# Performance work log

Measured on AMD Instinct MI355X. Metric: run time of the kernel, lower is better.

## Reference

```python
import jax, jax.numpy as jnp
import numpy as np

B, L, V, D, N, K = 8, 512, 50257, 1024, 1024, 256


def setup_inputs() -> dict:
    key = jax.random.key(0)
    ks = jax.random.split(key, 8)
    s = 0.02
    return {
        "input_ids": jax.random.randint(ks[0], (B, L), 0, V, dtype=jnp.int32),
        "emb_inp": jax.random.normal(ks[1], (V, D), jnp.float32) * s,
        "W_ih": jax.random.normal(ks[2], (3 * D, D), jnp.float32) * s,   # rows ordered [r|z|n] like torch GRU
        "W_hh": jax.random.normal(ks[3], (3 * D, D), jnp.float32) * s,
        "b_ih": jnp.zeros((3 * D,), jnp.float32),
        "b_hh": jnp.zeros((3 * D,), jnp.float32),
        "W_A": jax.random.normal(ks[4], (N * K, D), jnp.float32) * s,    # ctx_to_A weight
        "b_A": jnp.zeros((N * K,), jnp.float32),
        "emb_geom": jax.random.normal(ks[5], (V, N), jnp.float32) * s,
    }


def reference(input_ids, emb_inp, W_ih, W_hh, b_ih, b_hh, W_A, b_A, emb_geom):
    # token embedding: (B, L, D)
    x = emb_inp[input_ids]
    # precompute input-side GRU gates once: (B, L, 3D)
    gi = jnp.einsum('bld,gd->blg', x, W_ih) + b_ih

    def step(h, gi_t):
        gh = h @ W_hh.T + b_hh                       # (B, 3D)
        ir, iz, i_n = jnp.split(gi_t, 3, axis=-1)
        hr, hz, h_n = jnp.split(gh, 3, axis=-1)
        r = jax.nn.sigmoid(ir + hr)
        z = jax.nn.sigmoid(iz + hz)
        n = jnp.tanh(i_n + r * h_n)
        h_new = (1.0 - z) * n + z * h                # torch GRU update
        return h_new, None

    h0 = jnp.zeros((x.shape[0], D), x.dtype)
    ctx_vec, _ = jax.lax.scan(step, h0, jnp.swapaxes(gi, 0, 1))  # final hidden (B, D)

    # context -> subspace basis U: (B, n, k)
    U = (ctx_vec @ W_A.T + b_A).reshape(-1, N, K)

    # scores[b,v] = e_v^T (U U^T) e_v == ||U^T e_v||^2  (rank-k rewrite, same math)
    Ue = jnp.einsum('vn,bnk->bvk', emb_geom, U)      # (B, V, K)
    logits = jnp.sum(Ue * Ue, axis=-1)               # (B, V)
    return logits
```

## Files before the change

### kernel.cpp

```cpp
#include <hip/hip_runtime.h>

#define D 1024
#define G3 3072
#define NV 50257
#define NU 1024
#define KU 256
#define TOKROWS 4096
#define SCL 256.0f
#define ISCL2 (1.0f / 65536.0f)
#define ISCL4 (1.0f / 4294967296.0f)

typedef __attribute__((ext_vector_type(8))) _Float16 half8;
typedef __attribute__((ext_vector_type(4))) _Float16 half4;
typedef __attribute__((ext_vector_type(4))) float f32x4;
typedef __attribute__((ext_vector_type(4))) unsigned u32x4;

#define GLDS16(gp, lp) __builtin_amdgcn_global_load_lds( \
    (const __attribute__((address_space(1))) void*)(const void*)(gp), \
    (__attribute__((address_space(3))) void*)(void*)(lp), 16, 0, 0)

static __device__ __forceinline__ float sigmoidf_(float x) {
  return 1.0f / (1.0f + __expf(-x));
}
static __device__ __forceinline__ float tanhf_(float x) {
  float e = __expf(2.0f * x);
  return 1.0f - 2.0f / (e + 1.0f);
}

__global__ __launch_bounds__(256) void k_prep(
    const int* __restrict__ ids, const float* __restrict__ emb,
    const float* __restrict__ Wih,
    _Float16* __restrict__ xh, _Float16* __restrict__ xl,
    _Float16* __restrict__ wh, _Float16* __restrict__ wl)
{
  int t = threadIdx.x;
  int wg = blockIdx.x;
  const float* src;
  _Float16 *dh, *dl;
  if (wg < TOKROWS) {
    src = emb + (size_t)ids[wg] * D;
    dh = xh + (size_t)wg * D; dl = xl + (size_t)wg * D;
  } else {
    int r = wg - TOKROWS;
    src = Wih + (size_t)r * D;
    dh = wh + (size_t)r * D; dl = wl + (size_t)r * D;
  }
  f32x4 v = ((const f32x4*)src)[t];
  half4 h, l;
#pragma unroll
  for (int j = 0; j < 4; ++j) {
    float vs = v[j] * SCL;
    _Float16 hi = (_Float16)vs;
    h[j] = hi;
    l[j] = (_Float16)(vs - (float)hi);
  }
  *(half4*)(dh + t * 4) = h;
  *(half4*)(dl + t * 4) = l;
}

__global__ __launch_bounds__(256) void k_gi(
    const _Float16* __restrict__ Ah, const _Float16* __restrict__ Al,
    const _Float16* __restrict__ Bh, const _Float16* __restrict__ Bl,
    const float* __restrict__ bih, float* __restrict__ gi)
{
  __shared__ _Float16 Ash[128 * 64];
  __shared__ _Float16 Asl[128 * 64];
  __shared__ _Float16 Bsh[128 * 64];
  __shared__ _Float16 Bsl[128 * 64];
  int tid = threadIdx.x;
  int bm = blockIdx.x, bn = blockIdx.y;
  int lane = tid & 63, w = tid >> 6;
  int nl = lane & 15, q = lane >> 4;
  int wr = w >> 1, wc = w & 1;
  f32x4 zero = {0.f, 0.f, 0.f, 0.f};
  f32x4 acc[4][4];
#pragma unroll
  for (int i = 0; i < 4; i++)
#pragma unroll
    for (int j = 0; j < 4; j++) acc[i][j] = zero;
  int srow_in = tid >> 3;
  int cg = ((tid & 7) ^ (srow_in & 7)) * 8;
  for (int kc = 0; kc < 16; ++kc) {
    __syncthreads();
#pragma unroll
    for (int s = 0; s < 4; ++s) {
      size_t go = ((size_t)(bm * 128 + s * 32 + srow_in)) * D + kc * 64 + cg;
      size_t go2 = ((size_t)(bn * 128 + s * 32 + srow_in)) * D + kc * 64 + cg;
      int lb = s * 2048 + w * 512;
      GLDS16(Ah + go, Ash + lb);
      GLDS16(Al + go, Asl + lb);
      GLDS16(Bh + go2, Bsh + lb);
      GLDS16(Bl + go2, Bsl + lb);
    }
    __syncthreads();
    half8 afh[4][2], afl[4][2], bfh[4][2], bfl[4][2];
#pragma unroll
    for (int mt = 0; mt < 4; ++mt) {
      int R = wr * 64 + mt * 16 + nl;
#pragma unroll
      for (int kt = 0; kt < 2; ++kt) {
        int o = R * 64 + ((kt * 4 + q) ^ (R & 7)) * 8;
        afh[mt][kt] = *(const half8*)(Ash + o);
        afl[mt][kt] = *(const half8*)(Asl + o);
      }
    }
#pragma unroll
    for (int nt = 0; nt < 4; ++nt) {
      int R = wc * 64 + nt * 16 + nl;
#pragma unroll
      for (int kt = 0; kt < 2; ++kt) {
        int o = R * 64 + ((kt * 4 + q) ^ (R & 7)) * 8;
        bfh[nt][kt] = *(const half8*)(Bsh + o);
        bfl[nt][kt] = *(const half8*)(Bsl + o);
      }
    }
#pragma unroll
    for (int mt = 0; mt < 4; ++mt)
#pragma unroll
      for (int nt = 0; nt < 4; ++nt)
#pragma unroll
        for (int kt = 0; kt < 2; ++kt) {
          acc[mt][nt] = __builtin_amdgcn_mfma_f32_16x16x32_f16(afh[mt][kt], bfh[nt][kt], acc[mt][nt], 0, 0, 0);
          acc[mt][nt] = __builtin_amdgcn_mfma_f32_16x16x32_f16(afh[mt][kt], bfl[nt][kt], acc[mt][nt], 0, 0, 0);
          acc[mt][nt] = __builtin_amdgcn_mfma_f32_16x16x32_f16(afl[mt][kt], bfh[nt][kt], acc[mt][nt], 0, 0, 0);
        }
  }
#pragma unroll
  for (int mt = 0; mt < 4; ++mt)
#pragma unroll
    for (int nt = 0; nt < 4; ++nt) {
      int col = bn * 128 + wc * 64 + nt * 16 + nl;
      float bv = bih[col];
#pragma unroll
      for (int i = 0; i < 4; i++) {
        int row = bm * 128 + wr * 64 + mt * 16 + q * 4 + i;
        gi[(size_t)row * G3 + col] = acc[mt][nt][i] * ISCL2 + bv;
      }
    }
}

__global__ void k_init(unsigned* __restrict__ rec32)
{
  int t = threadIdx.x;
  for (int i = t; i < 32768; i += 256) rec32[i] = 0u;
}

__global__ __launch_bounds__(384) void k_gru(
    const float* __restrict__ Whh, const float* __restrict__ gi,
    const float* __restrict__ bhh, unsigned* __restrict__ hrec,
    float* __restrict__ ctx)
{
  int tid = threadIdx.x;
  int wid = blockIdx.x;
  int w = tid >> 6;
  int g = w >> 1;
  int kh = w & 1;
  int lane = tid & 63, nl = lane & 15, q = lane >> 4;
  __shared__ _Float16 hs[16 * 1024];
  __shared__ float gp[6][3][8][17];

  half8 bwh[16], bwl[16];
  {
    const float* wrow = Whh + ((size_t)(g * 1024 + wid * 16 + nl)) * D + kh * 512;
#pragma unroll
    for (int kt = 0; kt < 16; ++kt) {
      const f32x4* p = (const f32x4*)(wrow + kt * 32 + q * 8);
      f32x4 v0 = p[0], v1 = p[1];
      half8 h, l;
#pragma unroll
      for (int j = 0; j < 4; ++j) {
        float s0 = v0[j] * SCL;
        _Float16 h0 = (_Float16)s0;
        h[j] = h0; l[j] = (_Float16)(s0 - (float)h0);
        float s1 = v1[j] * SCL;
        _Float16 h1 = (_Float16)s1;
        h[j + 4] = h1; l[j + 4] = (_Float16)(s1 - (float)h1);
      }
      bwh[kt] = h; bwl[kt] = l;
    }
  }

  int m = tid >> 3, np = (tid & 7) * 2;
  int d0 = wid * 16 + np;
  float hr0 = 0.f, hr1 = 0.f;
  float bh[6] = {0, 0, 0, 0, 0, 0};
  if (tid < 64) {
#pragma unroll
    for (int gg = 0; gg < 3; ++gg) {
      bh[gg * 2] = bhh[gg * 1024 + d0];
      bh[gg * 2 + 1] = bhh[gg * 1024 + d0 + 1];
    }
  }
  f32x4 zero = {0, 0, 0, 0};

  for (int step = 0; step < 512; ++step) {
    float gi6[6] = {0, 0, 0, 0, 0, 0};
    if (tid < 64) {
      const float* gpt = gi + ((size_t)(m * 512 + step)) * G3 + d0;
#pragma unroll
      for (int gg = 0; gg < 3; ++gg) {
        gi6[gg * 2] = gpt[gg * 1024];
        gi6[gg * 2 + 1] = gpt[gg * 1024 + 1];
      }
    }

    {
      unsigned want = (unsigned)step;
      const u32x4* rb = (const u32x4*)hrec + (size_t)(step & 1) * 4096;
      u32x4 rv[11];
      unsigned need = 0;
#pragma unroll
      for (int k = 0; k < 11; ++k) {
        int r = tid + k * 384;
        if (r < 4096) need |= (1u << k);
      }
      while (need) {
        unsigned mm = need;
#pragma unroll
        for (int k = 0; k < 11; ++k)
          if (mm & (1u << k)) {
            int r = tid + k * 384;
            asm volatile("global_load_dwordx4 %0, %1, off sc0 sc1"
                         : "=v"(rv[k]) : "v"(rb + r));
          }
        asm volatile("s_waitcnt vmcnt(0)" ::: "memory");
#pragma unroll
        for (int k = 0; k < 11; ++k)
          if ((mm & (1u << k)) && rv[k][2] == want) need &= ~(1u << k);
      }
      __builtin_amdgcn_sched_barrier(0);
#pragma unroll
      for (int k = 0; k < 11; ++k) {
        int r = tid + k * 384;
        if (r < 4096) {
          int w2 = r >> 6, l2 = r & 63;
          int m2 = l2 >> 3;
          int d = (w2 << 4) + ((l2 & 7) << 1);
          int chunk = d >> 3, wi = d & 7;
          int sw = chunk ^ (m2 & 7);
          *(unsigned*)&hs[((m2 * 128 + sw) << 3) + wi] = rv[k][0];
          *(unsigned*)&hs[(((m2 + 8) * 128 + sw) << 3) + wi] = rv[k][1];
        }
      }
    }
    __syncthreads();

    half8 av[16];
#pragma unroll
    for (int kt = 0; kt < 16; ++kt) {
      int chunk = kh * 64 + kt * 4 + q;
      av[kt] = *(const half8*)&hs[(size_t)(nl * 128 + (chunk ^ (nl & 7))) * 8];
    }
    f32x4 ac1 = zero, ac2 = zero;
#pragma unroll
    for (int kt = 0; kt < 16; ++kt) {
      ac1 = __builtin_amdgcn_mfma_f32_16x16x32_f16(av[kt], bwh[kt], ac1, 0, 0, 0);
      ac2 = __builtin_amdgcn_mfma_f32_16x16x32_f16(av[kt], bwl[kt], ac2, 0, 0, 0);
    }
    if (q < 2) {
#pragma unroll
      for (int i = 0; i < 4; i++) {
        gp[w][0][q * 4 + i][nl] = ac1[i];
        gp[w][2][q * 4 + i][nl] = ac2[i];
      }
    } else {
#pragma unroll
      for (int i = 0; i < 4; i++) gp[w][1][(q - 2) * 4 + i][nl] = ac1[i];
    }
    __syncthreads();
    if (tid < 64) {
      float gh[6];
#pragma unroll
      for (int g2 = 0; g2 < 3; ++g2) {
        float s0 = 0.f, s1 = 0.f;
#pragma unroll
        for (int k2 = 0; k2 < 2; ++k2) {
          int wv = g2 * 2 + k2;
#pragma unroll
          for (int s = 0; s < 3; ++s) {
            s0 += gp[wv][s][m][np];
            s1 += gp[wv][s][m][np + 1];
          }
        }
        gh[g2 * 2] = s0 * ISCL2;
        gh[g2 * 2 + 1] = s1 * ISCL2;
      }
      float r0_ = sigmoidf_(gi6[0] + gh[0] + bh[0]);
      float r1_ = sigmoidf_(gi6[1] + gh[1] + bh[1]);
      float z0_ = sigmoidf_(gi6[2] + gh[2] + bh[2]);
      float z1_ = sigmoidf_(gi6[3] + gh[3] + bh[3]);
      float n0_ = tanhf_(gi6[4] + r0_ * (gh[4] + bh[4]));
      float n1_ = tanhf_(gi6[5] + r1_ * (gh[5] + bh[5]));
      float h0_ = (1.f - z0_) * n0_ + z0_ * hr0;
      float h1_ = (1.f - z1_) * n1_ + z1_ * hr1;
      hr0 = h0_; hr1 = h1_;
      float s0 = h0_ * SCL, s1 = h1_ * SCL;
      _Float16 h0h = (_Float16)s0, h1h = (_Float16)s1;
      _Float16 h0l = (_Float16)(s0 - (float)h0h), h1l = (_Float16)(s1 - (float)h1h);
      u32x4 rec;
      rec[0] = (unsigned)__builtin_bit_cast(unsigned short, h0h) |
               ((unsigned)__builtin_bit_cast(unsigned short, h1h) << 16);
      rec[1] = (unsigned)__builtin_bit_cast(unsigned short, h0l) |
               ((unsigned)__builtin_bit_cast(unsigned short, h1l) << 16);
      rec[2] = (unsigned)(step + 1);
      rec[3] = 0u;
      u32x4* dst = (u32x4*)hrec + ((size_t)((step + 1) & 1) * 4096 + wid * 64 + tid);
      asm volatile("global_store_dwordx4 %0, %1, off sc0 sc1"
                   :: "v"(dst), "v"(rec) : "memory");
      if (step == 511) {
        ctx[m * D + d0] = h0_;
        ctx[m * D + d0 + 1] = h1_;
      }
    }
  }
}

__global__ __launch_bounds__(256) void k_u(
    const float* __restrict__ WA, const float* __restrict__ bA,
    const float* __restrict__ ctx, _Float16* __restrict__ Uth,
    _Float16* __restrict__ Utl)
{
  __shared__ float As[128 * 32];
  __shared__ float cx[8][1032];
  int tid = threadIdx.x;
  int RB = blockIdx.x;
#pragma unroll
  for (int jj = 0; jj < 8; ++jj) {
    int e = tid * 32 + jj * 4;
    *(f32x4*)&cx[e >> 10][e & 1023] = *(const f32x4*)(ctx + e);
  }
  float acc[4] = {0.f, 0.f, 0.f, 0.f};
  int b = tid & 7, rq = tid >> 3;
  float* AsW = As + (tid >> 6) * 256;
  int sr = tid >> 3;
  int sc = (tid & 7) * 4;
  __syncthreads();
  for (int kc = 0; kc < 32; ++kc) {
    __syncthreads();
    const float* gsrc = WA + ((size_t)(RB * 128 + sr)) * D + kc * 32 + sc;
    GLDS16(gsrc, AsW);
    GLDS16(gsrc + 32 * D, AsW + 1024);
    GLDS16(gsrc + 64 * D, AsW + 2048);
    GLDS16(gsrc + 96 * D, AsW + 3072);
    __syncthreads();
    f32x4 cxr[8];
#pragma unroll
    for (int kk = 0; kk < 8; ++kk) cxr[kk] = *(const f32x4*)&cx[b][kc * 32 + kk * 4];
#pragma unroll
    for (int r = 0; r < 4; ++r) {
      const float* ap = As + (rq * 4 + r) * 32;
      float s = 0.f;
#pragma unroll
      for (int kk = 0; kk < 8; ++kk) {
        f32x4 a = *(const f32x4*)(ap + kk * 4);
        f32x4 c = cxr[kk];
        s += a[0] * c[0] + a[1] * c[1] + a[2] * c[2] + a[3] * c[3];
      }
      acc[r] += s;
    }
  }
#pragma unroll
  for (int r = 0; r < 4; ++r) {
    int R = RB * 128 + rq * 4 + r;
    float v = (acc[r] + bA[R]) * SCL;
    int n_u = R >> 8, k_u = R & 255;
    _Float16 hi = (_Float16)v;
    size_t o = ((size_t)(b * 256 + k_u)) * NU + n_u;
    Uth[o] = hi;
    Utl[o] = (_Float16)(v - (float)hi);
  }
}

__global__ __launch_bounds__(512, 2) void k_logits(
    const float* __restrict__ eg, const _Float16* __restrict__ Uth,
    const _Float16* __restrict__ Utl, float* __restrict__ out)
{
  __shared__ _Float16 Ash[128 * 40];
  __shared__ _Float16 Asl[128 * 40];
  __shared__ float lacc[8][128];
  int tid = threadIdx.x;
  int v0 = blockIdx.x * 128;
  int lane = tid & 63, w = tid >> 6, nl = lane & 15, q = lane >> 4;
  int bq = w & 3, wk = w >> 2;
  for (int i = tid; i < 1024; i += 512) ((float*)lacc)[i] = 0.f;
  int sr = tid >> 2;
  int sc = (tid & 3) * 8;
  int vr = v0 + sr;
  if (vr >= NV) vr = NV - 1;
  const float* asrc = eg + (size_t)vr * NU;
  f32x4 zero = {0, 0, 0, 0};
  __syncthreads();
  for (int kg = 0; kg < 8; ++kg) {
    f32x4 acc[2][8];
#pragma unroll
    for (int b = 0; b < 2; ++b)
#pragma unroll
      for (int mt = 0; mt < 8; ++mt) acc[b][mt] = zero;
    for (int nc = 0; nc < 32; ++nc) {
      __syncthreads();
      {
        const f32x4* p = (const f32x4*)(asrc + nc * 32 + sc);
        f32x4 u0 = p[0];
        f32x4 u1 = p[1];
        half8 h, l;
#pragma unroll
        for (int j = 0; j < 4; ++j) {
          float s0 = u0[j] * SCL;
          _Float16 h0 = (_Float16)s0;
          h[j] = h0; l[j] = (_Float16)(s0 - (float)h0);
          float s1 = u1[j] * SCL;
          _Float16 h1 = (_Float16)s1;
          h[j + 4] = h1; l[j + 4] = (_Float16)(s1 - (float)h1);
        }
        *(half8*)(Ash + sr * 40 + sc) = h;
        *(half8*)(Asl + sr * 40 + sc) = l;
      }
      __syncthreads();
      half8 bfh0, bfl0, bfh1, bfl1;
      {
        int bb0 = bq * 2;
        size_t o0 = ((size_t)(bb0 * 256 + kg * 32 + wk * 16 + nl)) * NU + nc * 32 + q * 8;
        size_t o1 = o0 + (size_t)256 * NU;
        bfh0 = *(const half8*)(Uth + o0);
        bfl0 = *(const half8*)(Utl + o0);
        bfh1 = *(const half8*)(Uth + o1);
        bfl1 = *(const half8*)(Utl + o1);
      }
      __builtin_amdgcn_s_setprio(1);
#pragma unroll
      for (int c = 0; c < 2; ++c) {
        half8 afh[4], afl[4];
#pragma unroll
        for (int mt = 0; mt < 4; ++mt) {
          int row = (c * 4 + mt) * 16 + nl;
          afh[mt] = *(const half8*)(Ash + row * 40 + q * 8);
          afl[mt] = *(const half8*)(Asl + row * 40 + q * 8);
        }
#pragma unroll
        for (int mt = 0; mt < 4; ++mt) {
          int g = c * 4 + mt;
          acc[0][g] = __builtin_amdgcn_mfma_f32_16x16x32_f16(afh[mt], bfh0, acc[0][g], 0, 0, 0);
          acc[0][g] = __builtin_amdgcn_mfma_f32_16x16x32_f16(afh[mt], bfl0, acc[0][g], 0, 0, 0);
          acc[0][g] = __builtin_amdgcn_mfma_f32_16x16x32_f16(afl[mt], bfh0, acc[0][g], 0, 0, 0);
          acc[1][g] = __builtin_amdgcn_mfma_f32_16x16x32_f16(afh[mt], bfh1, acc[1][g], 0, 0, 0);
          acc[1][g] = __builtin_amdgcn_mfma_f32_16x16x32_f16(afh[mt], bfl1, acc[1][g], 0, 0, 0);
          acc[1][g] = __builtin_amdgcn_mfma_f32_16x16x32_f16(afl[mt], bfh1, acc[1][g], 0, 0, 0);
        }
      }
      __builtin_amdgcn_s_setprio(0);
    }
#pragma unroll
    for (int b = 0; b < 2; ++b) {
      int bb = bq * 2 + b;
#pragma unroll
      for (int mt = 0; mt < 8; ++mt) {
#pragma unroll
        for (int i = 0; i < 4; ++i) {
          float s = acc[b][mt][i] * acc[b][mt][i];
          s += __shfl_xor(s, 1);
          s += __shfl_xor(s, 2);
          s += __shfl_xor(s, 4);
          s += __shfl_xor(s, 8);
          if (nl == 0) atomicAdd(&lacc[bb][mt * 16 + q * 4 + i], s);
        }
      }
    }
  }
  __syncthreads();
  if (tid < 128) {
    int v = v0 + tid;
    if (v < NV) {
#pragma unroll
      for (int b = 0; b < 8; ++b) out[(size_t)b * NV + v] = lacc[b][tid] * ISCL4;
    }
  }
}

extern "C" void kernel_launch(void* const* d_in, const int* in_sizes, int n_in,
                              void* d_out, int out_size, void* d_ws, size_t ws_size,
                              hipStream_t stream)
{
  (void)in_sizes; (void)n_in; (void)out_size; (void)ws_size;
  const int* ids = (const int*)d_in[0];
  const float* emb = (const float*)d_in[1];
  const float* Wih = (const float*)d_in[2];
  const float* Whh = (const float*)d_in[3];
  const float* bih = (const float*)d_in[4];
  const float* bhh = (const float*)d_in[5];
  const float* WA = (const float*)d_in[6];
  const float* bA = (const float*)d_in[7];
  const float* eg = (const float*)d_in[8];
  float* out = (float*)d_out;

  char* ws = (char*)d_ws;
  size_t off = 0;
  auto take = [&](size_t bytes) -> char* {
    char* p = ws + off;
    off += (bytes + 255) & ~(size_t)255;
    return p;
  };
  float* gi32 = (float*)take((size_t)4096 * 3072 * 4);
  char* xregion = take((size_t)4096 * 1024 * 2 * 2);
  _Float16* xh = (_Float16*)xregion;
  _Float16* xl = xh + (size_t)4096 * 1024;
  _Float16* wh = (_Float16*)take((size_t)3072 * 1024 * 2);
  _Float16* wl = (_Float16*)take((size_t)3072 * 1024 * 2);
  unsigned* hrec = (unsigned*)take((size_t)2 * 4096 * 16);
  float* ctx = (float*)take((size_t)8 * 1024 * 4);
  _Float16* Uth = (_Float16*)xregion;
  _Float16* Utl = Uth + (size_t)8 * 256 * 1024;

  k_prep<<<dim3(7168), dim3(256), 0, stream>>>(ids, emb, Wih, xh, xl, wh, wl);
  k_gi<<<dim3(32, 24), dim3(256), 0, stream>>>(xh, xl, wh, wl, bih, gi32);
  k_init<<<dim3(1), dim3(256), 0, stream>>>(hrec);
  k_gru<<<dim3(64), dim3(384), 0, stream>>>(Whh, gi32, bhh, hrec, ctx);
  k_u<<<dim3(2048), dim3(256), 0, stream>>>(WA, bA, ctx, Uth, Utl);
  k_logits<<<dim3(393), dim3(512), 0, stream>>>(eg, Uth, Utl, out);
}
```

Baseline: 2.964 ms.

## Register-prefetch next tile of emb_geom and U in k_logits main loop

Loads the next iteration's emb_geom slice and U fragments into registers while the current tile is converted and multiplied, so global load latency overlaps the MFMA work. Barriers now wait only on LDS (lgkmcnt) rather than all memory, so the in-flight prefetches do not stall them. Launch bounds are relaxed from 2 to 1 blocks per CU to make room for the extra live registers, which may lower occupancy.

Measured after the change: 3.064 ms. +3.4%, slower.

```diff
diff --git a/kernel.cpp b/kernel.cpp
--- a/kernel.cpp
+++ b/kernel.cpp
@@ -18,6 +18,12 @@
 #define GLDS16(gp, lp) __builtin_amdgcn_global_load_lds( \
     (const __attribute__((address_space(1))) void*)(const void*)(gp), \
     (__attribute__((address_space(3))) void*)(void*)(lp), 16, 0, 0)
+
+#define LBAR() do { \
+    asm volatile("s_waitcnt lgkmcnt(0)" ::: "memory"); \
+    __builtin_amdgcn_s_barrier(); \
+    __builtin_amdgcn_sched_barrier(0); \
+  } while (0)
 
 static __device__ __forceinline__ float sigmoidf_(float x) {
   return 1.0f / (1.0f + __expf(-x));
@@ -371,7 +377,7 @@
   }
 }
 
-__global__ __launch_bounds__(512, 2) void k_logits(
+__global__ __launch_bounds__(512, 1) void k_logits(
     const float* __restrict__ eg, const _Float16* __restrict__ Uth,
     const _Float16* __restrict__ Utl, float* __restrict__ out)
 {
@@ -389,7 +395,15 @@
   if (vr >= NV) vr = NV - 1;
   const float* asrc = eg + (size_t)vr * NU;
   f32x4 zero = {0, 0, 0, 0};
-  __syncthreads();
+  int bb0 = bq * 2;
+  f32x4 eu0 = *(const f32x4*)(asrc + sc);
+  f32x4 eu1 = *(const f32x4*)(asrc + sc + 4);
+  size_t ob = ((size_t)(bb0 * 256 + wk * 16 + nl)) * NU + q * 8;
+  half8 pbh0 = *(const half8*)(Uth + ob);
+  half8 pbl0 = *(const half8*)(Utl + ob);
+  half8 pbh1 = *(const half8*)(Uth + ob + (size_t)256 * NU);
+  half8 pbl1 = *(const half8*)(Utl + ob + (size_t)256 * NU);
+
   for (int kg = 0; kg < 8; ++kg) {
     f32x4 acc[2][8];
 #pragma unroll
@@ -397,35 +411,37 @@
 #pragma unroll
       for (int mt = 0; mt < 8; ++mt) acc[b][mt] = zero;
     for (int nc = 0; nc < 32; ++nc) {
-      __syncthreads();
+      LBAR();
+      f32x4 ceu0 = eu0, ceu1 = eu1;
+      half8 bh0 = pbh0, bl0 = pbl0, bh1 = pbh1, bl1 = pbl1;
       {
-        const f32x4* p = (const f32x4*)(asrc + nc * 32 + sc);
-        f32x4 u0 = p[0];
-        f32x4 u1 = p[1];
         half8 h, l;
 #pragma unroll
         for (int j = 0; j < 4; ++j) {
-          float s0 = u0[j] * SCL;
+          float s0 = ceu0[j] * SCL;
           _Float16 h0 = (_Float16)s0;
           h[j] = h0; l[j] = (_Float16)(s0 - (float)h0);
-          float s1 = u1[j] * SCL;
+          float s1 = ceu1[j] * SCL;
           _Float16 h1 = (_Float16)s1;
           h[j + 4] = h1; l[j + 4] = (_Float16)(s1 - (float)h1);
         }
         *(half8*)(Ash + sr * 40 + sc) = h;
         *(half8*)(Asl + sr * 40 + sc) = l;
       }
-      __syncthreads();
-      half8 bfh0, bfl0, bfh1, bfl1;
       {
-        int bb0 = bq * 2;
-        size_t o0 = ((size_t)(bb0 * 256 + kg * 32 + wk * 16 + nl)) * NU + nc * 32 + q * 8;
-        size_t o1 = o0 + (size_t)256 * NU;
-        bfh0 = *(const half8*)(Uth + o0);
-        bfl0 = *(const half8*)(Utl + o0);
-        bfh1 = *(const half8*)(Uth + o1);
-        bfl1 = *(const half8*)(Utl + o1);
-      }
+        int t = kg * 32 + nc;
+        int tn = t + 1 < 255 ? t + 1 : 255;
+        int kgn = tn >> 5, ncn = tn & 31;
+        const f32x4* np_ = (const f32x4*)(asrc + ncn * 32 + sc);
+        eu0 = np_[0];
+        eu1 = np_[1];
+        size_t on = ((size_t)(bb0 * 256 + kgn * 32 + wk * 16 + nl)) * NU + ncn * 32 + q * 8;
+        pbh0 = *(const half8*)(Uth + on);
+        pbl0 = *(const half8*)(Utl + on);
+        pbh1 = *(const half8*)(Uth + on + (size_t)256 * NU);
+        pbl1 = *(const half8*)(Utl + on + (size_t)256 * NU);
+      }
+      LBAR();
       __builtin_amdgcn_s_setprio(1);
 #pragma unroll
       for (int c = 0; c < 2; ++c) {
@@ -439,12 +455,12 @@
 #pragma unroll
         for (int mt = 0; mt < 4; ++mt) {
           int g = c * 4 + mt;
-          acc[0][g] = __builtin_amdgcn_mfma_f32_16x16x32_f16(afh[mt], bfh0, acc[0][g], 0, 0, 0);
-          acc[0][g] = __builtin_amdgcn_mfma_f32_16x16x32_f16(afh[mt], bfl0, acc[0][g], 0, 0, 0);
-          acc[0][g] = __builtin_amdgcn_mfma_f32_16x16x32_f16(afl[mt], bfh0, acc[0][g], 0, 0, 0);
-          acc[1][g] = __builtin_amdgcn_mfma_f32_16x16x32_f16(afh[mt], bfh1, acc[1][g], 0, 0, 0);
-          acc[1][g] = __builtin_amdgcn_mfma_f32_16x16x32_f16(afh[mt], bfl1, acc[1][g], 0, 0, 0);
-          acc[1][g] = __builtin_amdgcn_mfma_f32_16x16x32_f16(afl[mt], bfh1, acc[1][g], 0, 0, 0);
+          acc[0][g] = __builtin_amdgcn_mfma_f32_16x16x32_f16(afh[mt], bh0, acc[0][g], 0, 0, 0);
+          acc[0][g] = __builtin_amdgcn_mfma_f32_16x16x32_f16(afh[mt], bl0, acc[0][g], 0, 0, 0);
+          acc[0][g] = __builtin_amdgcn_mfma_f32_16x16x32_f16(afl[mt], bh0, acc[0][g], 0, 0, 0);
+          acc[1][g] = __builtin_amdgcn_mfma_f32_16x16x32_f16(afh[mt], bh1, acc[1][g], 0, 0, 0);
+          acc[1][g] = __builtin_amdgcn_mfma_f32_16x16x32_f16(afh[mt], bl1, acc[1][g], 0, 0, 0);
+          acc[1][g] = __builtin_amdgcn_mfma_f32_16x16x32_f16(afl[mt], bh1, acc[1][g], 0, 0, 0);
         }
       }
       __builtin_amdgcn_s_setprio(0);
```

## Retile logits kernel to 256 vocab rows per block, one batch per wave

Applied to the files above, without the earlier changes.

The logits kernel now stages 256 vocabulary rows per block instead of 128. Each of the 8 waves owns one batch element and loops over all 16 K-groups, so each wave loads one U fragment pair per step instead of two. Because each wave now owns its batch row in the shared accumulator, the shared-memory atomicAdd becomes a plain add. In exchange, emb_geom is re-read and re-split to fp16 twice as many times per row, and the grid shrinks to 197 blocks, which may leave compute units idle.

Measured after the change: 3.361 ms. 13.4% more time.

```diff
diff --git a/kernel.cpp b/kernel.cpp
--- a/kernel.cpp
+++ b/kernel.cpp
@@ -375,60 +375,57 @@
     const float* __restrict__ eg, const _Float16* __restrict__ Uth,
     const _Float16* __restrict__ Utl, float* __restrict__ out)
 {
-  __shared__ _Float16 Ash[128 * 40];
-  __shared__ _Float16 Asl[128 * 40];
-  __shared__ float lacc[8][128];
+  __shared__ _Float16 Ash[256 * 40];
+  __shared__ _Float16 Asl[256 * 40];
+  __shared__ float lacc[8][256];
   int tid = threadIdx.x;
-  int v0 = blockIdx.x * 128;
+  int v0 = blockIdx.x * 256;
   int lane = tid & 63, w = tid >> 6, nl = lane & 15, q = lane >> 4;
-  int bq = w & 3, wk = w >> 2;
-  for (int i = tid; i < 1024; i += 512) ((float*)lacc)[i] = 0.f;
-  int sr = tid >> 2;
-  int sc = (tid & 3) * 8;
+  for (int i = tid; i < 2048; i += 512) ((float*)lacc)[i] = 0.f;
+  int sr = tid >> 1;
+  int sc = (tid & 1) * 16;
   int vr = v0 + sr;
   if (vr >= NV) vr = NV - 1;
   const float* asrc = eg + (size_t)vr * NU;
   f32x4 zero = {0, 0, 0, 0};
   __syncthreads();
-  for (int kg = 0; kg < 8; ++kg) {
-    f32x4 acc[2][8];
-#pragma unroll
-    for (int b = 0; b < 2; ++b)
-#pragma unroll
-      for (int mt = 0; mt < 8; ++mt) acc[b][mt] = zero;
+  for (int kg = 0; kg < 16; ++kg) {
+    f32x4 acc[16];
+#pragma unroll
+    for (int mt = 0; mt < 16; ++mt) acc[mt] = zero;
     for (int nc = 0; nc < 32; ++nc) {
       __syncthreads();
       {
         const f32x4* p = (const f32x4*)(asrc + nc * 32 + sc);
-        f32x4 u0 = p[0];
-        f32x4 u1 = p[1];
-        half8 h, l;
+        f32x4 u0 = p[0], u1 = p[1], u2 = p[2], u3 = p[3];
+        half8 h0v, l0v, h1v, l1v;
 #pragma unroll
         for (int j = 0; j < 4; ++j) {
           float s0 = u0[j] * SCL;
-          _Float16 h0 = (_Float16)s0;
-          h[j] = h0; l[j] = (_Float16)(s0 - (float)h0);
+          _Float16 a = (_Float16)s0;
+          h0v[j] = a; l0v[j] = (_Float16)(s0 - (float)a);
           float s1 = u1[j] * SCL;
-          _Float16 h1 = (_Float16)s1;
-          h[j + 4] = h1; l[j + 4] = (_Float16)(s1 - (float)h1);
+          _Float16 b = (_Float16)s1;
+          h0v[j + 4] = b; l0v[j + 4] = (_Float16)(s1 - (float)b);
+          float s2 = u2[j] * SCL;
+          _Float16 c = (_Float16)s2;
+          h1v[j] = c; l1v[j] = (_Float16)(s2 - (float)c);
+          float s3 = u3[j] * SCL;
+          _Float16 d = (_Float16)s3;
+          h1v[j + 4] = d; l1v[j + 4] = (_Float16)(s3 - (float)d);
         }
-        *(half8*)(Ash + sr * 40 + sc) = h;
-        *(half8*)(Asl + sr * 40 + sc) = l;
+        *(half8*)(Ash + sr * 40 + sc) = h0v;
+        *(half8*)(Asl + sr * 40 + sc) = l0v;
+        *(half8*)(Ash + sr * 40 + sc + 8) = h1v;
+        *(half8*)(Asl + sr * 40 + sc + 8) = l1v;
       }
       __syncthreads();
-      half8 bfh0, bfl0, bfh1, bfl1;
-      {
-        int bb0 = bq * 2;
-        size_t o0 = ((size_t)(bb0 * 256 + kg * 32 + wk * 16 + nl)) * NU + nc * 32 + q * 8;
-        size_t o1 = o0 + (size_t)256 * NU;
-        bfh0 = *(const half8*)(Uth + o0);
-        bfl0 = *(const half8*)(Utl + o0);
-        bfh1 = *(const half8*)(Uth + o1);
-        bfl1 = *(const half8*)(Utl + o1);
-      }
+      size_t o = ((size_t)(w * 256 + kg * 16 + nl)) * NU + nc * 32 + q * 8;
+      half8 bfh = *(const half8*)(Uth + o);
+      half8 bfl = *(const half8*)(Utl + o);
       __builtin_amdgcn_s_setprio(1);
 #pragma unroll
-      for (int c = 0; c < 2; ++c) {
+      for (int c = 0; c < 4; ++c) {
         half8 afh[4], afl[4];
 #pragma unroll
         for (int mt = 0; mt < 4; ++mt) {
@@ -439,35 +436,28 @@
 #pragma unroll
         for (int mt = 0; mt < 4; ++mt) {
           int g = c * 4 + mt;
-          acc[0][g] = __builtin_amdgcn_mfma_f32_16x16x32_f16(afh[mt], bfh0, acc[0][g], 0, 0, 0);
-          acc[0][g] = __builtin_amdgcn_mfma_f32_16x16x32_f16(afh[mt], bfl0, acc[0][g], 0, 0, 0);
-          acc[0][g] = __builtin_amdgcn_mfma_f32_16x16x32_f16(afl[mt], bfh0, acc[0][g], 0, 0, 0);
-          acc[1][g] = __builtin_amdgcn_mfma_f32_16x16x32_f16(afh[mt], bfh1, acc[1][g], 0, 0, 0);
-          acc[1][g] = __builtin_amdgcn_mfma_f32_16x16x32_f16(afh[mt], bfl1, acc[1][g], 0, 0, 0);
-          acc[1][g] = __builtin_amdgcn_mfma_f32_16x16x32_f16(afl[mt], bfh1, acc[1][g], 0, 0, 0);
+          acc[g] = __builtin_amdgcn_mfma_f32_16x16x32_f16(afh[mt], bfh, acc[g], 0, 0, 0);
+          acc[g] = __builtin_amdgcn_mfma_f32_16x16x32_f16(afh[mt], bfl, acc[g], 0, 0, 0);
+          acc[g] = __builtin_amdgcn_mfma_f32_16x16x32_f16(afl[mt], bfh, acc[g], 0, 0, 0);
         }
       }
       __builtin_amdgcn_s_setprio(0);
     }
 #pragma unroll
-    for (int b = 0; b < 2; ++b) {
-      int bb = bq * 2 + b;
-#pragma unroll
-      for (int mt = 0; mt < 8; ++mt) {
-#pragma unroll
-        for (int i = 0; i < 4; ++i) {
-          float s = acc[b][mt][i] * acc[b][mt][i];
-          s += __shfl_xor(s, 1);
-          s += __shfl_xor(s, 2);
-          s += __shfl_xor(s, 4);
-          s += __shfl_xor(s, 8);
-          if (nl == 0) atomicAdd(&lacc[bb][mt * 16 + q * 4 + i], s);
-        }
+    for (int mt = 0; mt < 16; ++mt) {
+#pragma unroll
+      for (int i = 0; i < 4; ++i) {
+        float s = acc[mt][i] * acc[mt][i];
+        s += __shfl_xor(s, 1);
+        s += __shfl_xor(s, 2);
+        s += __shfl_xor(s, 4);
+        s += __shfl_xor(s, 8);
+        if (nl == 0) lacc[w][mt * 16 + q * 4 + i] += s;
       }
     }
   }
   __syncthreads();
-  if (tid < 128) {
+  if (tid < 256) {
     int v = v0 + tid;
     if (v < NV) {
 #pragma unroll
@@ -515,5 +505,5 @@
   k_init<<<dim3(1), dim3(256), 0, stream>>>(hrec);
   k_gru<<<dim3(64), dim3(384), 0, stream>>>(Whh, gi32, bhh, hrec, ctx);
   k_u<<<dim3(2048), dim3(256), 0, stream>>>(WA, bA, ctx, Uth, Utl);
-  k_logits<<<dim3(393), dim3(512), 0, stream>>>(eg, Uth, Utl, out);
-}
+  k_logits<<<dim3(197), dim3(512), 0, stream>>>(eg, Uth, Utl, out);
+}
```
